# Performance work log

Measured on AMD Instinct MI355X. Metric: run time of the kernel, lower is better.

The kernel has to match this reference:

```python
import jax, jax.numpy as jnp
import numpy as np
import math

S, D, H, DK, F = 4096, 1024, 16, 64, 4096
EPS = 1e-5

def _layernorm(x, g, b):
    mu = jnp.mean(x, axis=-1, keepdims=True)
    var = jnp.mean(jnp.square(x - mu), axis=-1, keepdims=True)
    return (x - mu) * jax.lax.rsqrt(var + EPS) * g + b

def setup_inputs() -> dict:
    key = jax.random.key(0)
    ks = jax.random.split(key, 12)
    s = 0.02
    return {
        "src": jax.random.normal(ks[0], (S, D), jnp.float32),
        "Wq": jax.random.normal(ks[1], (H, D, DK), jnp.float32) * s,
        "bq": jnp.zeros((H, DK), jnp.float32),
        "Wk": jax.random.normal(ks[2], (H, D, DK), jnp.float32) * s,
        "bk": jnp.zeros((H, DK), jnp.float32),
        "Wv": jax.random.normal(ks[3], (H, D, DK), jnp.float32) * s,
        "bv": jnp.zeros((H, DK), jnp.float32),
        "Wo": jax.random.normal(ks[4], (H * DK, D), jnp.float32) * s,
        "bo": jnp.zeros((D,), jnp.float32),
        "ln1_g": jnp.ones((D,), jnp.float32),
        "ln1_b": jnp.zeros((D,), jnp.float32),
        "W1": jax.random.normal(ks[5], (D, F), jnp.float32) * s,
        "b1": jnp.zeros((F,), jnp.float32),
        "W2": jax.random.normal(ks[6], (F, D), jnp.float32) * s,
        "b2": jnp.zeros((D,), jnp.float32),
        "ln2_g": jnp.ones((D,), jnp.float32),
        "ln2_b": jnp.zeros((D,), jnp.float32),
    }

def reference(src, Wq, bq, Wk, bk, Wv, bv, Wo, bo, ln1_g, ln1_b,
              W1, b1, W2, b2, ln2_g, ln2_b):
    # per-head projections, batched over heads: [H, S, DK]
    q = jnp.einsum('sd,hdk->hsk', src, Wq) + bq[:, None, :]
    k = jnp.einsum('sd,hdk->hsk', src, Wk) + bk[:, None, :]
    v = jnp.einsum('sd,hdk->hsk', src, Wv) + bv[:, None, :]
    logits = jnp.einsum('hsk,htk->hst', q, k) / math.sqrt(DK)  # [H, S, S]
    attn = jax.nn.softmax(logits, axis=-1)
    vals = jnp.einsum('hst,htk->hsk', attn, v)                 # [H, S, DK]
    concat = jnp.transpose(vals, (1, 0, 2)).reshape(S, H * DK) # cat along features
    attn_out = concat @ Wo + bo
    x1 = _layernorm(src + attn_out, ln1_g, ln1_b)
    ffn = jnp.maximum(x1 @ W1 + b1, 0.0) @ W2 + b2
    return _layernorm(x1 + ffn, ln2_g, ln2_b)
```

## Files before the change

### kernel.cpp

```cpp
#include <hip/hip_runtime.h>
#include <hip/hip_bf16.h>

#define S_ 4096
#define D_ 1024
#define H_ 16
#define DK_ 64
#define F_ 4096

typedef short bf16x8_t __attribute__((ext_vector_type(8)));
typedef float f32x4_t __attribute__((ext_vector_type(4)));

#define MFMA16(a, b, c) __builtin_amdgcn_mfma_f32_16x16x32_bf16(a, b, c, 0, 0, 0)

#define QSCALE 0.1803368801111243f

__device__ __forceinline__ short f2bf(float f) {
  union { float f; unsigned u; } a; a.f = f;
  unsigned r = a.u + 0x7fffu + ((a.u >> 16) & 1u);
  return (short)(r >> 16);
}
__device__ __forceinline__ float bf2f(short s) {
  union { unsigned u; float f; } a; a.u = ((unsigned)(unsigned short)s) << 16;
  return a.f;
}
__device__ __forceinline__ unsigned cvtpk_bf16(float lo, float hi) {
  unsigned w;
  asm("v_cvt_pk_bf16_f32 %0, %1, %2" : "=v"(w) : "v"(lo), "v"(hi));
  return w;
}
__device__ __forceinline__ float exp2_fast(float x) {
  float r;
  asm("v_exp_f32 %0, %1" : "=v"(r) : "v"(x));
  return r;
}

__device__ __forceinline__ void async_copy16(short* ldsDst, const short* gSrc) {
  __builtin_amdgcn_global_load_lds(
      (const __attribute__((address_space(1))) unsigned int*)gSrc,
      (__attribute__((address_space(3))) unsigned int*)ldsDst, 16, 0, 0);
}

template<int HEADMODE>
__global__ __launch_bounds__(256)
void prep_w(const float* __restrict__ W, short* __restrict__ outHi, int K, int N) {
  __shared__ float t[32][33];
  int n0 = blockIdx.x * 32, k0 = blockIdx.y * 32;
  int tid = threadIdx.x;
  int cin = tid & 31, kin = tid >> 5;
#pragma unroll
  for (int i = 0; i < 4; ++i) {
    int k = kin + i * 8;
    int n = n0 + cin;
    long srcIdx;
    if (HEADMODE) srcIdx = ((long)(n >> 6) * K + (k0 + k)) * 64 + (n & 63);
    else          srcIdx = (long)(k0 + k) * N + n;
    t[k][cin] = W[srcIdx];
  }
  __syncthreads();
  int kout = tid & 31, cb = tid >> 5;
#pragma unroll
  for (int i = 0; i < 4; ++i) {
    int c = cb + i * 8;
    outHi[(long)(n0 + c) * K + (k0 + kout)] = f2bf(t[kout][c]);
  }
}

__global__ __launch_bounds__(256)
void cvt_b(const float* __restrict__ x, short* __restrict__ h) {
  long i = ((long)blockIdx.x * 256 + threadIdx.x) * 4;
  float4 v = *(const float4*)(x + i);
  short4 hh;
  hh.x = f2bf(v.x);
  hh.y = f2bf(v.y);
  hh.z = f2bf(v.z);
  hh.w = f2bf(v.w);
  *(short4*)(h + i) = hh;
}

#define EPI_QKV 0
#define EPI_PART 1
#define EPI_RELUHL 2

template<int AHL, int EPI, int SPLITK>
__global__ __launch_bounds__(256)
void gemm_bf(const short* __restrict__ AH, const short* __restrict__ AL,
             const short* __restrict__ BH,
             int K, int M, int N,
             const float* __restrict__ bq_, const float* __restrict__ bk_,
             const float* __restrict__ bv_,
             void* __restrict__ out0, void* __restrict__ out1) {
  constexpr int NP = AHL ? 3 : 2;
  __shared__ short lds[NP * 4096];
  const int m0 = blockIdx.x * 128, n0 = blockIdx.y * 128;
  const int tid = threadIdx.x;
  const int wave = tid >> 6, lane = tid & 63;
  const int wr = wave >> 1, wc = wave & 1;
  const int lg = lane >> 4, lr = lane & 15;
  const int kLen = (SPLITK > 1) ? (K / SPLITK) : K;
  const long kBase = (SPLITK > 1) ? (long)blockIdx.z * kLen : 0;
  const int nk = kLen >> 5;

  const short* gAH = AH + (long)m0 * K + kBase;
  const short* gAL = AHL ? (AL + (long)m0 * K + kBase) : nullptr;
  const short* gBH = BH + (long)n0 * K + kBase;

  f32x4_t acc[4][4];
#pragma unroll
  for (int i = 0; i < 4; ++i)
#pragma unroll
    for (int j = 0; j < 4; ++j)
      acc[i][j] = (f32x4_t){0.f, 0.f, 0.f, 0.f};

  for (int kt = 0; kt < nk; ++kt) {
#pragma unroll
    for (int p = 0; p < 2 * NP; ++p) {
      const short* gb;
      if constexpr (AHL) gb = (p < 2) ? gAH : (p < 4) ? gAL : gBH;
      else               gb = (p < 2) ? gAH : gBH;
      int w = ((p & 1) << 8) | tid;
      int row = w >> 2;
      int gsw = ((w & 3) ^ (row & 3)) << 3;
      async_copy16(lds + (((p << 8) | tid) << 3),
                   gb + (long)row * K + (kt << 5) + gsw);
    }
    __syncthreads();
    bf16x8_t ah[4], al[4], bh[4];
    constexpr int BOFF = AHL ? 8192 : 4096;
#pragma unroll
    for (int f = 0; f < 4; ++f) {
      int ar = wr * 64 + f * 16 + lr;
      int ag = (lg ^ (ar & 3)) << 3;
      ah[f] = *(const bf16x8_t*)(lds + ar * 32 + ag);
      if constexpr (AHL) al[f] = *(const bf16x8_t*)(lds + 4096 + ar * 32 + ag);
      int br = wc * 64 + f * 16 + lr;
      int bg = (lg ^ (br & 3)) << 3;
      bh[f] = *(const bf16x8_t*)(lds + BOFF + br * 32 + bg);
    }
#pragma unroll
    for (int i = 0; i < 4; ++i)
#pragma unroll
      for (int j = 0; j < 4; ++j) {
        acc[i][j] = MFMA16(ah[i], bh[j], acc[i][j]);
        if constexpr (AHL) acc[i][j] = MFMA16(al[i], bh[j], acc[i][j]);
      }
    __syncthreads();
  }

#pragma unroll
  for (int i = 0; i < 4; ++i) {
    int mB = m0 + wr * 64 + i * 16 + lg * 4;
#pragma unroll
    for (int j = 0; j < 4; ++j) {
      int n = n0 + wc * 64 + j * 16 + lr;
      if constexpr (EPI == EPI_PART) {
        float* outp = (float*)out0 + (long)blockIdx.z * M * N;
#pragma unroll
        for (int r = 0; r < 4; ++r)
          outp[(long)(mB + r) * N + n] = acc[i][j][r];
      } else if constexpr (EPI == EPI_RELUHL) {
        float bs = bq_[n];
        short* oH = (short*)out0;
        short* oL = (short*)out1;
#pragma unroll
        for (int r = 0; r < 4; ++r) {
          float v = fmaxf(acc[i][j][r] + bs, 0.f);
          short hi = f2bf(v);
          long idx = (long)(mB + r) * N + n;
          oH[idx] = hi;
          oL[idx] = f2bf(v - bf2f(hi));
        }
      } else {
        short* qko = (short*)out0;
        short* vto = (short*)out1;
        if (n < 1024) {
          float bs = bq_[n];
#pragma unroll
          for (int r = 0; r < 4; ++r)
            qko[(long)(mB + r) * 2048 + n] = f2bf((acc[i][j][r] + bs) * QSCALE);
        } else if (n < 2048) {
          float bs = bk_[n - 1024];
#pragma unroll
          for (int r = 0; r < 4; ++r)
            qko[(long)(mB + r) * 2048 + n] = f2bf(acc[i][j][r] + bs);
        } else {
          float bs = bv_[n - 2048];
          short4 pk;
          pk.x = f2bf(acc[i][j][0] + bs);
          pk.y = f2bf(acc[i][j][1] + bs);
          pk.z = f2bf(acc[i][j][2] + bs);
          pk.w = f2bf(acc[i][j][3] + bs);
          *(short4*)(vto + (long)(n - 2048) * S_ + mB) = pk;
        }
      }
    }
  }
}

__global__ __launch_bounds__(256, 2)
void attn_kernel(const short* __restrict__ qk, const short* __restrict__ vT,
                 short* __restrict__ attnB) {
  __shared__ short kvlds[2][2][4096];
  __shared__ short plds[4][32][72];
  const int qt = blockIdx.x, h = blockIdx.y;
  const int tid = threadIdx.x;
  const int wave = tid >> 6, lane = tid & 63;
  const int lg = lane >> 4, lr = lane & 15;
  const int qrow0 = qt * 128 + wave * 32;

  const short* qh = qk + (long)qrow0 * 2048 + h * 64;
  const short* kh = qk + 1024 + h * 64;
  const short* vh = vT + (long)h * 64 * S_;

  bf16x8_t qf[2][2];
#pragma unroll
  for (int qb = 0; qb < 2; ++qb)
#pragma unroll
    for (int di = 0; di < 2; ++di)
      qf[qb][di] = *(const bf16x8_t*)(qh + (long)(qb * 16 + lr) * 2048 + di * 32 + lg * 8);

  float m[2] = {-1e30f, -1e30f}, l[2] = {0.f, 0.f};
  f32x4_t o[2][4];
#pragma unroll
  for (int qb = 0; qb < 2; ++qb)
#pragma unroll
    for (int dd = 0; dd < 4; ++dd) o[qb][dd] = (f32x4_t){0.f, 0.f, 0.f, 0.f};

  auto stage = [&](int buf, int kt) {
    short* kd = &kvlds[buf][0][0];
    short* vd = &kvlds[buf][1][0];
    const long kt64 = (long)kt * 64;
#pragma unroll
    for (int p = 0; p < 2; ++p) {
      int idx = tid + p * 256;
      int row = idx >> 3, c = idx & 7;
      int csw = (c ^ (row & 7)) << 3;
      async_copy16(kd + idx * 8, kh + (kt64 + row) * 2048 + csw);
      async_copy16(vd + idx * 8, vh + (long)row * S_ + kt64 + csw);
    }
  };

  stage(0, 0);
  __syncthreads();

  for (int kt = 0; kt < S_ / 64; ++kt) {
    const int buf = kt & 1;
    if (kt + 1 < S_ / 64) stage(buf ^ 1, kt + 1);

    const short* Kb = &kvlds[buf][0][0];
    const short* Vb = &kvlds[buf][1][0];

    bf16x8_t kf[8];
#pragma unroll
    for (int kc = 0; kc < 4; ++kc)
#pragma unroll
      for (int di = 0; di < 2; ++di)
        kf[kc * 2 + di] = *(const bf16x8_t*)(
            Kb + ((kc * 16 + lr) << 6) + (((di * 4 + lg) ^ (lr & 7)) << 3));

    f32x4_t sacc[2][4];
#pragma unroll
    for (int qb = 0; qb < 2; ++qb)
#pragma unroll
      for (int kc = 0; kc < 4; ++kc) sacc[qb][kc] = (f32x4_t){0.f, 0.f, 0.f, 0.f};
    __builtin_amdgcn_s_setprio(1);
#pragma unroll
    for (int kc = 0; kc < 4; ++kc)
#pragma unroll
      for (int qb = 0; qb < 2; ++qb) {
        sacc[qb][kc] = MFMA16(kf[kc * 2 + 0], qf[qb][0], sacc[qb][kc]);
        sacc[qb][kc] = MFMA16(kf[kc * 2 + 1], qf[qb][1], sacc[qb][kc]);
      }
    __builtin_amdgcn_s_setprio(0);

#pragma unroll
    for (int qb = 0; qb < 2; ++qb) {
      float p01 = fmaxf(fmaxf(sacc[qb][0][0], sacc[qb][0][1]),
                        fmaxf(sacc[qb][0][2], sacc[qb][0][3]));
      float p23 = fmaxf(fmaxf(sacc[qb][1][0], sacc[qb][1][1]),
                        fmaxf(sacc[qb][1][2], sacc[qb][1][3]));
      float p45 = fmaxf(fmaxf(sacc[qb][2][0], sacc[qb][2][1]),
                        fmaxf(sacc[qb][2][2], sacc[qb][2][3]));
      float p67 = fmaxf(fmaxf(sacc[qb][3][0], sacc[qb][3][1]),
                        fmaxf(sacc[qb][3][2], sacc[qb][3][3]));
      float pmax = fmaxf(fmaxf(p01, p23), fmaxf(p45, p67));
      pmax = fmaxf(pmax, __shfl_xor(pmax, 16));
      pmax = fmaxf(pmax, __shfl_xor(pmax, 32));
      if (!__all(pmax <= m[qb] + 8.0f)) {
        float ef = exp2_fast(m[qb] - pmax);
        m[qb] = pmax;
        l[qb] *= ef;
#pragma unroll
        for (int dd = 0; dd < 4; ++dd) o[qb][dd] *= ef;
      }
      float mq = m[qb];
      float rsum = 0.f;
#pragma unroll
      for (int kc = 0; kc < 4; ++kc) {
        float e0 = exp2_fast(sacc[qb][kc][0] - mq);
        float e1 = exp2_fast(sacc[qb][kc][1] - mq);
        float e2 = exp2_fast(sacc[qb][kc][2] - mq);
        float e3 = exp2_fast(sacc[qb][kc][3] - mq);
        rsum += (e0 + e1) + (e2 + e3);
        uint2 w;
        w.x = cvtpk_bf16(e0, e1);
        w.y = cvtpk_bf16(e2, e3);
        *(uint2*)&plds[wave][qb * 16 + lr][kc * 16 + lg * 4] = w;
      }
      rsum += __shfl_xor(rsum, 16);
      rsum += __shfl_xor(rsum, 32);
      l[qb] += rsum;
    }

    bf16x8_t pb[2][2];
#pragma unroll
    for (int qb = 0; qb < 2; ++qb)
#pragma unroll
      for (int ks = 0; ks < 2; ++ks)
        pb[qb][ks] = *(const bf16x8_t*)&plds[wave][qb * 16 + lr][ks * 32 + lg * 8];

    bf16x8_t vf[8];
#pragma unroll
    for (int dd = 0; dd < 4; ++dd)
#pragma unroll
      for (int ks = 0; ks < 2; ++ks)
        vf[dd * 2 + ks] = *(const bf16x8_t*)(
            Vb + ((dd * 16 + lr) << 6) + (((ks * 4 + lg) ^ (lr & 7)) << 3));

    __builtin_amdgcn_s_setprio(1);
#pragma unroll
    for (int dd = 0; dd < 4; ++dd)
#pragma unroll
      for (int qb = 0; qb < 2; ++qb) {
        o[qb][dd] = MFMA16(vf[dd * 2 + 0], pb[qb][0], o[qb][dd]);
        o[qb][dd] = MFMA16(vf[dd * 2 + 1], pb[qb][1], o[qb][dd]);
      }
    __builtin_amdgcn_s_setprio(0);

    __syncthreads();
  }

#pragma unroll
  for (int qb = 0; qb < 2; ++qb) {
    float inv = 1.0f / l[qb];
    int q = qrow0 + qb * 16 + lr;
#pragma unroll
    for (int dd = 0; dd < 4; ++dd) {
      long base = (long)q * D_ + h * 64 + dd * 16 + lg * 4;
      short4 hh;
      hh.x = f2bf(o[qb][dd][0] * inv);
      hh.y = f2bf(o[qb][dd][1] * inv);
      hh.z = f2bf(o[qb][dd][2] * inv);
      hh.w = f2bf(o[qb][dd][3] * inv);
      *(short4*)(attnB + base) = hh;
    }
  }
}

template<int WB>
__global__ __launch_bounds__(256)
void ln_fused(const float* __restrict__ pA, const float* __restrict__ pB,
              const float* __restrict__ res, const float* __restrict__ bias,
              const float* __restrict__ g, const float* __restrict__ b,
              float* __restrict__ outF, short* __restrict__ outB) {
  __shared__ float red[8];
  const int row = blockIdx.x, tid = threadIdx.x;
  const long base = (long)row * D_ + tid * 4;
  float4 a = *(const float4*)(pA + base);
  float4 c = *(const float4*)(pB + base);
  float4 rr = *(const float4*)(res + base);
  float4 bb = *(const float4*)(bias + tid * 4);
  float x0 = a.x + c.x + rr.x + bb.x;
  float x1v = a.y + c.y + rr.y + bb.y;
  float x2v = a.z + c.z + rr.z + bb.z;
  float x3v = a.w + c.w + rr.w + bb.w;
  float s = x0 + x1v + x2v + x3v;
  float s2 = x0 * x0 + x1v * x1v + x2v * x2v + x3v * x3v;
#pragma unroll
  for (int m = 1; m < 64; m <<= 1) {
    s += __shfl_xor(s, m);
    s2 += __shfl_xor(s2, m);
  }
  int wave = tid >> 6, lane = tid & 63;
  if (lane == 0) { red[wave * 2] = s; red[wave * 2 + 1] = s2; }
  __syncthreads();
  s = red[0] + red[2] + red[4] + red[6];
  s2 = red[1] + red[3] + red[5] + red[7];
  float mu = s * (1.f / D_);
  float var = s2 * (1.f / D_) - mu * mu;
  float rs = rsqrtf(var + 1e-5f);
  float4 gv = *(const float4*)(g + tid * 4);
  float4 bv = *(const float4*)(b + tid * 4);
  float y0 = (x0 - mu) * rs * gv.x + bv.x;
  float y1 = (x1v - mu) * rs * gv.y + bv.y;
  float y2 = (x2v - mu) * rs * gv.z + bv.z;
  float y3 = (x3v - mu) * rs * gv.w + bv.w;
  float4 ov = {y0, y1, y2, y3};
  *(float4*)(outF + base) = ov;
  if constexpr (WB) {
    short4 hh;
    hh.x = f2bf(y0);
    hh.y = f2bf(y1);
    hh.z = f2bf(y2);
    hh.w = f2bf(y3);
    *(short4*)(outB + base) = hh;
  }
}

extern "C" void kernel_launch(void* const* d_in, const int* in_sizes, int n_in,
                              void* d_out, int out_size, void* d_ws, size_t ws_size,
                              hipStream_t stream) {
  const float* src  = (const float*)d_in[0];
  const float* Wq   = (const float*)d_in[1];
  const float* bq   = (const float*)d_in[2];
  const float* Wk   = (const float*)d_in[3];
  const float* bk   = (const float*)d_in[4];
  const float* Wv   = (const float*)d_in[5];
  const float* bv   = (const float*)d_in[6];
  const float* Wo   = (const float*)d_in[7];
  const float* bo   = (const float*)d_in[8];
  const float* ln1g = (const float*)d_in[9];
  const float* ln1b = (const float*)d_in[10];
  const float* W1   = (const float*)d_in[11];
  const float* b1   = (const float*)d_in[12];
  const float* W2   = (const float*)d_in[13];
  const float* b2   = (const float*)d_in[14];
  const float* ln2g = (const float*)d_in[15];
  const float* ln2b = (const float*)d_in[16];
  float* out = (float*)d_out;

  const size_t SD = (size_t)S_ * D_;
  const size_t SF = (size_t)S_ * F_;

  char* w = (char*)d_ws;
  auto take = [&](size_t bytes) {
    char* p = w;
    w += (bytes + 255) & ~(size_t)255;
    return p;
  };
  short* srcB  = (short*)take(SD * 2);
  short* qkb   = (short*)take((size_t)S_ * 2048 * 2);
  short* vTb   = (short*)take((size_t)D_ * S_ * 2);
  short* h1H   = (short*)take(SF * 2);
  short* h1L   = (short*)take(SF * 2);
  short* wqkvB = (short*)take((size_t)3072 * D_ * 2);
  short* woB   = (short*)take((size_t)D_ * D_ * 2);
  short* w1B   = (short*)take((size_t)F_ * D_ * 2);
  short* w2B   = (short*)take((size_t)D_ * F_ * 2);
  short* attnB = (short*)take(SD * 2);
  float* x1    = (float*)take(SD * 4);
  short* x1B   = (short*)take(SD * 2);

  float* partWo = (float*)h1H;
  float* partW2 = (float*)srcB;

  dim3 blk(256);

  prep_w<1><<<dim3(32, 32), blk, 0, stream>>>(Wq, wqkvB, D_, D_);
  prep_w<1><<<dim3(32, 32), blk, 0, stream>>>(Wk, wqkvB + (size_t)1024 * D_, D_, D_);
  prep_w<1><<<dim3(32, 32), blk, 0, stream>>>(Wv, wqkvB + (size_t)2048 * D_, D_, D_);
  prep_w<0><<<dim3(32, 32), blk, 0, stream>>>(Wo, woB, D_, D_);
  prep_w<0><<<dim3(128, 32), blk, 0, stream>>>(W1, w1B, D_, F_);
  prep_w<0><<<dim3(32, 128), blk, 0, stream>>>(W2, w2B, F_, D_);

  cvt_b<<<dim3(4096), blk, 0, stream>>>(src, srcB);

  gemm_bf<0, EPI_QKV, 1><<<dim3(32, 24), blk, 0, stream>>>(
      srcB, nullptr, wqkvB, D_, S_, 3072, bq, bk, bv, qkb, vTb);

  attn_kernel<<<dim3(32, 16), blk, 0, stream>>>(qkb, vTb, attnB);

  gemm_bf<0, EPI_PART, 2><<<dim3(32, 8, 2), blk, 0, stream>>>(
      attnB, nullptr, woB, D_, S_, D_, nullptr, nullptr, nullptr, partWo, nullptr);
  ln_fused<1><<<dim3(S_), blk, 0, stream>>>(partWo, partWo + SD, src, bo,
                                            ln1g, ln1b, x1, x1B);

  gemm_bf<0, EPI_RELUHL, 1><<<dim3(32, 32), blk, 0, stream>>>(
      x1B, nullptr, w1B, D_, S_, F_, b1, nullptr, nullptr, h1H, h1L);
  gemm_bf<1, EPI_PART, 2><<<dim3(32, 8, 2), blk, 0, stream>>>(
      h1H, h1L, w2B, F_, S_, D_, nullptr, nullptr, nullptr, partW2, nullptr);
  ln_fused<0><<<dim3(S_), blk, 0, stream>>>(partW2, partW2 + SD, x1, b2,
                                            ln2g, ln2b, out, nullptr);

  (void)in_sizes; (void)n_in; (void)out_size; (void)ws_size;
}
```

Measured before the change: 486.4 us.

## Drop hi/lo split for FFN hidden and software-pipeline attention QK with softmax/PV

The FFN hidden activation is now stored as a single bf16 tensor instead of a hi/lo bf16 pair, so the W2 GEMM loads one A operand and issues half the MFMAs. The attention loop is restructured into a two-stage software pipeline: the QK^T MFMAs for the next key tile and its V fragment loads are issued before the softmax and PV of the current tile, using double sets of score and V registers. The precision drop on the hidden activation may loosen accuracy. The pipelining raises register pressure in the attention kernel.

```diff
diff --git a/kernel.cpp b/kernel.cpp
--- a/kernel.cpp
+++ b/kernel.cpp
@@ -79,18 +79,16 @@
 
 #define EPI_QKV 0
 #define EPI_PART 1
-#define EPI_RELUHL 2
-
-template<int AHL, int EPI, int SPLITK>
+#define EPI_RELUB 2
+
+template<int EPI, int SPLITK>
 __global__ __launch_bounds__(256)
-void gemm_bf(const short* __restrict__ AH, const short* __restrict__ AL,
-             const short* __restrict__ BH,
+void gemm_bf(const short* __restrict__ AH, const short* __restrict__ BH,
              int K, int M, int N,
              const float* __restrict__ bq_, const float* __restrict__ bk_,
              const float* __restrict__ bv_,
              void* __restrict__ out0, void* __restrict__ out1) {
-  constexpr int NP = AHL ? 3 : 2;
-  __shared__ short lds[NP * 4096];
+  __shared__ short lds[8192];
   const int m0 = blockIdx.x * 128, n0 = blockIdx.y * 128;
   const int tid = threadIdx.x;
   const int wave = tid >> 6, lane = tid & 63;
@@ -101,7 +99,6 @@
   const int nk = kLen >> 5;
 
   const short* gAH = AH + (long)m0 * K + kBase;
-  const short* gAL = AHL ? (AL + (long)m0 * K + kBase) : nullptr;
   const short* gBH = BH + (long)n0 * K + kBase;
 
   f32x4_t acc[4][4];
@@ -113,10 +110,8 @@
 
   for (int kt = 0; kt < nk; ++kt) {
 #pragma unroll
-    for (int p = 0; p < 2 * NP; ++p) {
-      const short* gb;
-      if constexpr (AHL) gb = (p < 2) ? gAH : (p < 4) ? gAL : gBH;
-      else               gb = (p < 2) ? gAH : gBH;
+    for (int p = 0; p < 4; ++p) {
+      const short* gb = (p < 2) ? gAH : gBH;
       int w = ((p & 1) << 8) | tid;
       int row = w >> 2;
       int gsw = ((w & 3) ^ (row & 3)) << 3;
@@ -124,25 +119,21 @@
                    gb + (long)row * K + (kt << 5) + gsw);
     }
     __syncthreads();
-    bf16x8_t ah[4], al[4], bh[4];
-    constexpr int BOFF = AHL ? 8192 : 4096;
+    bf16x8_t ah[4], bh[4];
 #pragma unroll
     for (int f = 0; f < 4; ++f) {
       int ar = wr * 64 + f * 16 + lr;
       int ag = (lg ^ (ar & 3)) << 3;
       ah[f] = *(const bf16x8_t*)(lds + ar * 32 + ag);
-      if constexpr (AHL) al[f] = *(const bf16x8_t*)(lds + 4096 + ar * 32 + ag);
       int br = wc * 64 + f * 16 + lr;
       int bg = (lg ^ (br & 3)) << 3;
-      bh[f] = *(const bf16x8_t*)(lds + BOFF + br * 32 + bg);
+      bh[f] = *(const bf16x8_t*)(lds + 4096 + br * 32 + bg);
     }
 #pragma unroll
     for (int i = 0; i < 4; ++i)
 #pragma unroll
-      for (int j = 0; j < 4; ++j) {
+      for (int j = 0; j < 4; ++j)
         acc[i][j] = MFMA16(ah[i], bh[j], acc[i][j]);
-        if constexpr (AHL) acc[i][j] = MFMA16(al[i], bh[j], acc[i][j]);
-      }
     __syncthreads();
   }
 
@@ -157,18 +148,12 @@
 #pragma unroll
         for (int r = 0; r < 4; ++r)
           outp[(long)(mB + r) * N + n] = acc[i][j][r];
-      } else if constexpr (EPI == EPI_RELUHL) {
+      } else if constexpr (EPI == EPI_RELUB) {
         float bs = bq_[n];
-        short* oH = (short*)out0;
-        short* oL = (short*)out1;
-#pragma unroll
-        for (int r = 0; r < 4; ++r) {
-          float v = fmaxf(acc[i][j][r] + bs, 0.f);
-          short hi = f2bf(v);
-          long idx = (long)(mB + r) * N + n;
-          oH[idx] = hi;
-          oL[idx] = f2bf(v - bf2f(hi));
-        }
+        short* oB = (short*)out0;
+#pragma unroll
+        for (int r = 0; r < 4; ++r)
+          oB[(long)(mB + r) * N + n] = f2bf(fmaxf(acc[i][j][r] + bs, 0.f));
       } else {
         short* qko = (short*)out0;
         short* vto = (short*)out1;
@@ -239,16 +224,8 @@
     }
   };
 
-  stage(0, 0);
-  __syncthreads();
-
-  for (int kt = 0; kt < S_ / 64; ++kt) {
-    const int buf = kt & 1;
-    if (kt + 1 < S_ / 64) stage(buf ^ 1, kt + 1);
-
-    const short* Kb = &kvlds[buf][0][0];
-    const short* Vb = &kvlds[buf][1][0];
-
+  auto qkStep = [&](int kt, f32x4_t (&sacc)[2][4]) {
+    const short* Kb = &kvlds[kt & 1][0][0];
     bf16x8_t kf[8];
 #pragma unroll
     for (int kc = 0; kc < 4; ++kc)
@@ -256,8 +233,6 @@
       for (int di = 0; di < 2; ++di)
         kf[kc * 2 + di] = *(const bf16x8_t*)(
             Kb + ((kc * 16 + lr) << 6) + (((di * 4 + lg) ^ (lr & 7)) << 3));
-
-    f32x4_t sacc[2][4];
 #pragma unroll
     for (int qb = 0; qb < 2; ++qb)
 #pragma unroll
@@ -271,7 +246,19 @@
         sacc[qb][kc] = MFMA16(kf[kc * 2 + 1], qf[qb][1], sacc[qb][kc]);
       }
     __builtin_amdgcn_s_setprio(0);
-
+  };
+
+  auto vload = [&](int kt, bf16x8_t (&vf)[8]) {
+    const short* Vb = &kvlds[kt & 1][1][0];
+#pragma unroll
+    for (int dd = 0; dd < 4; ++dd)
+#pragma unroll
+      for (int ks = 0; ks < 2; ++ks)
+        vf[dd * 2 + ks] = *(const bf16x8_t*)(
+            Vb + ((dd * 16 + lr) << 6) + (((ks * 4 + lg) ^ (lr & 7)) << 3));
+  };
+
+  auto smStep = [&](f32x4_t (&sacc)[2][4]) {
 #pragma unroll
     for (int qb = 0; qb < 2; ++qb) {
       float p01 = fmaxf(fmaxf(sacc[qb][0][0], sacc[qb][0][1]),
@@ -310,22 +297,15 @@
       rsum += __shfl_xor(rsum, 32);
       l[qb] += rsum;
     }
-
+  };
+
+  auto pvStep = [&](bf16x8_t (&vf)[8]) {
     bf16x8_t pb[2][2];
 #pragma unroll
     for (int qb = 0; qb < 2; ++qb)
 #pragma unroll
       for (int ks = 0; ks < 2; ++ks)
         pb[qb][ks] = *(const bf16x8_t*)&plds[wave][qb * 16 + lr][ks * 32 + lg * 8];
-
-    bf16x8_t vf[8];
-#pragma unroll
-    for (int dd = 0; dd < 4; ++dd)
-#pragma unroll
-      for (int ks = 0; ks < 2; ++ks)
-        vf[dd * 2 + ks] = *(const bf16x8_t*)(
-            Vb + ((dd * 16 + lr) << 6) + (((ks * 4 + lg) ^ (lr & 7)) << 3));
-
     __builtin_amdgcn_s_setprio(1);
 #pragma unroll
     for (int dd = 0; dd < 4; ++dd)
@@ -335,7 +315,34 @@
         o[qb][dd] = MFMA16(vf[dd * 2 + 1], pb[qb][1], o[qb][dd]);
       }
     __builtin_amdgcn_s_setprio(0);
-
+  };
+
+  f32x4_t saccA[2][4], saccB[2][4];
+  bf16x8_t vfA[8], vfB[8];
+  constexpr int NT = S_ / 64;
+
+  stage(0, 0);
+  __syncthreads();
+  qkStep(0, saccA);
+  stage(1, 1);
+  vload(0, vfA);
+  __syncthreads();
+
+  for (int kt = 0; kt < NT; kt += 2) {
+    qkStep(kt + 1, saccB);
+    if (kt + 2 < NT) stage(kt & 1, kt + 2);
+    vload(kt + 1, vfB);
+    smStep(saccA);
+    pvStep(vfA);
+    __syncthreads();
+
+    if (kt + 2 < NT) {
+      qkStep(kt + 2, saccA);
+      if (kt + 3 < NT) stage((kt + 1) & 1, kt + 3);
+      vload(kt + 2, vfA);
+    }
+    smStep(saccB);
+    pvStep(vfB);
     __syncthreads();
   }
 
@@ -440,8 +447,7 @@
   short* srcB  = (short*)take(SD * 2);
   short* qkb   = (short*)take((size_t)S_ * 2048 * 2);
   short* vTb   = (short*)take((size_t)D_ * S_ * 2);
-  short* h1H   = (short*)take(SF * 2);
-  short* h1L   = (short*)take(SF * 2);
+  short* h1B   = (short*)take(SF * 2);
   short* wqkvB = (short*)take((size_t)3072 * D_ * 2);
   short* woB   = (short*)take((size_t)D_ * D_ * 2);
   short* w1B   = (short*)take((size_t)F_ * D_ * 2);
@@ -450,7 +456,7 @@
   float* x1    = (float*)take(SD * 4);
   short* x1B   = (short*)take(SD * 2);
 
-  float* partWo = (float*)h1H;
+  float* partWo = (float*)h1B;
   float* partW2 = (float*)srcB;
 
   dim3 blk(256);
@@ -464,20 +470,20 @@
 
   cvt_b<<<dim3(4096), blk, 0, stream>>>(src, srcB);
 
-  gemm_bf<0, EPI_QKV, 1><<<dim3(32, 24), blk, 0, stream>>>(
-      srcB, nullptr, wqkvB, D_, S_, 3072, bq, bk, bv, qkb, vTb);
+  gemm_bf<EPI_QKV, 1><<<dim3(32, 24), blk, 0, stream>>>(
+      srcB, wqkvB, D_, S_, 3072, bq, bk, bv, qkb, vTb);
 
   attn_kernel<<<dim3(32, 16), blk, 0, stream>>>(qkb, vTb, attnB);
 
-  gemm_bf<0, EPI_PART, 2><<<dim3(32, 8, 2), blk, 0, stream>>>(
-      attnB, nullptr, woB, D_, S_, D_, nullptr, nullptr, nullptr, partWo, nullptr);
+  gemm_bf<EPI_PART, 2><<<dim3(32, 8, 2), blk, 0, stream>>>(
+      attnB, woB, D_, S_, D_, nullptr, nullptr, nullptr, partWo, nullptr);
   ln_fused<1><<<dim3(S_), blk, 0, stream>>>(partWo, partWo + SD, src, bo,
                                             ln1g, ln1b, x1, x1B);
 
-  gemm_bf<0, EPI_RELUHL, 1><<<dim3(32, 32), blk, 0, stream>>>(
-      x1B, nullptr, w1B, D_, S_, F_, b1, nullptr, nullptr, h1H, h1L);
-  gemm_bf<1, EPI_PART, 2><<<dim3(32, 8, 2), blk, 0, stream>>>(
-      h1H, h1L, w2B, F_, S_, D_, nullptr, nullptr, nullptr, partW2, nullptr);
+  gemm_bf<EPI_RELUB, 1><<<dim3(32, 32), blk, 0, stream>>>(
+      x1B, w1B, D_, S_, F_, b1, nullptr, nullptr, h1B, nullptr);
+  gemm_bf<EPI_PART, 2><<<dim3(32, 8, 2), blk, 0, stream>>>(
+      h1B, w2B, F_, S_, D_, nullptr, nullptr, nullptr, partW2, nullptr);
   ln_fused<0><<<dim3(S_), blk, 0, stream>>>(partW2, partW2 + SD, x1, b2,
                                             ln2g, ln2b, out, nullptr);
 
```

Result: faster. 443.0 us (-8.9%).
